# Performance work log

Hardware: AMD Instinct MI355X
Metric: run time of the kernel (lower is better)

Reference implementation:

```python
import jax, jax.numpy as jnp
import numpy as np

B, L1, C, L2, S, N_DB, N_CLS = 8, 1024, 128, 256, 16, 8192, 128
EPS = 1e-8


def setup_inputs() -> dict:
    key = jax.random.key(0)
    k1, k2, k3, k4 = jax.random.split(key, 4)
    seq_input = jax.random.randint(k1, (B, L1), 0, C)                      # token ids
    kp_indices = jnp.sort(jax.random.randint(k2, (B, S + 1), 0, L1), axis=-1)  # sorted keypoint positions
    database = jax.random.normal(k3, (N_DB, C, L2), dtype=jnp.float32)     # stored normalised snapshots
    db_classes = jax.random.randint(k4, (N_DB,), 0, N_CLS)                 # class label per db snapshot
    return {"seq_input": seq_input, "kp_indices": kp_indices,
            "database": database, "db_classes": db_classes}


def _snapshots(seq_input, kp_indices):
    # encodeContinuousVarsAsBits: one-hot bit encoding -> (B, L1, C)
    encoded = jax.nn.one_hot(seq_input, C, dtype=jnp.float32)
    # keypoint segments [start, end) per sliding window, resampled to length L2
    starts = kp_indices[:, :-1]                                            # (B, S)
    ends = jnp.maximum(kp_indices[:, 1:], starts + 1)                      # ensure end > start
    frac = (jnp.arange(L2, dtype=jnp.float32) + 0.5) / L2                  # (L2,)
    pos = starts[..., None].astype(jnp.float32) + \
          (ends - starts)[..., None].astype(jnp.float32) * frac            # (B, S, L2)
    idx = jnp.clip(pos.astype(jnp.int32), 0, L1 - 1)                       # gather indices
    b_idx = jnp.arange(B)[:, None, None]
    snaps = encoded[b_idx, idx, :]                                         # (B, S, L2, C)
    snaps = jnp.transpose(snaps, (0, 1, 3, 2))                             # (B, S, C, L2)
    return snaps.reshape(B * S, C, L2)


def reference(seq_input, kp_indices, database, db_classes):
    snaps = _snapshots(seq_input, kp_indices)                              # (B*S, C, L2)
    # removeInvalidNormalisedSnapshots: zero-mask all-zero snapshots (jit-safe analogue)
    nz = jnp.any(snaps != 0, axis=(1, 2))
    snaps = snaps * nz[:, None, None].astype(snaps.dtype)
    # compare_1d_batches: cosine similarity of flattened snapshots vs database
    a = snaps.reshape(B * S, C * L2)
    a = a / (jnp.linalg.norm(a, axis=-1, keepdims=True) + EPS)
    d = database.reshape(N_DB, C * L2)
    d = d / (jnp.linalg.norm(d, axis=-1, keepdims=True) + EPS)
    sims = a @ d.T                                                          # (B*S, N_DB)
    top = jnp.argmax(sims, axis=-1)
    predictions = db_classes[top]                                           # top_cls
    unit_sim = jnp.max(sims, axis=-1)
    return sims, predictions, unit_sim
```

## Files before the change

kernel.cpp:

```cpp
#include <hip/hip_runtime.h>
#include <stdint.h>

constexpr int kB   = 8;
constexpr int kL1  = 1024;
constexpr int kC   = 128;
constexpr int kL2  = 256;
constexpr int kS   = 16;
constexpr int kNQ  = kB * kS;
constexpr int kNDB = 8192;
constexpr float kEPS = 1e-8f;
constexpr int kRow = kC * kL2;

constexpr int kGrid = 256;
constexpr int kGens = kNDB / kGrid;

#define BARRIER_LG()                                          \
    do {                                                      \
        asm volatile("s_waitcnt lgkmcnt(0)" ::: "memory");    \
        __builtin_amdgcn_s_barrier();                         \
        asm volatile("" ::: "memory");                        \
    } while (0)

__global__ void build_table_kernel(const int* __restrict__ seq,
                                   const int* __restrict__ kp,
                                   uint32_t* __restrict__ table) {
    __shared__ int csh[kL2];
    const int q = blockIdx.x;
    const int s0 = threadIdx.x;
    const int b = q >> 4;
    const int s = q & 15;
    int start = kp[b * (kS + 1) + s];
    int end_  = kp[b * (kS + 1) + s + 1];
    if (end_ < start + 1) end_ = start + 1;
    {
        const int l2 = s0;
        const float frac = (l2 + 0.5f) * (1.0f / 256.0f);
        const float pos = __fadd_rn((float)start,
                                    __fmul_rn((float)(end_ - start), frac));
        int idx = (int)pos;
        idx = idx < 0 ? 0 : (idx > kL1 - 1 ? kL1 - 1 : idx);
        csh[l2] = seq[b * kL1 + idx];
    }
    __syncthreads();
    const int h = s0 >> 6;
    const int g = s0 & 63;
    const int l2r = h * 64 + (((q & 63) + g) & 63);
    const int c = csh[l2r];
    table[(q * 4 + h) * 64 + g] = (uint32_t)((c * kL2 + l2r) * 4);
}

__launch_bounds__(1024, 1)
__global__ void sim_kernel(const float* __restrict__ db,
                           const uint32_t* __restrict__ table,
                           float* __restrict__ sims) {
    __shared__ float tile[kRow];
    __shared__ float accp[2][3][128];
    __shared__ float nshp[2][8];

    const int blk  = blockIdx.x;
    const int row0 = blk * kGens;
    const int t = threadIdx.x;

    if (t < 512) {
        const int p = t;
        const float* rp = db + (size_t)row0 * kRow;
        float4 buf[16];
        #pragma unroll
        for (int k = 0; k < 16; ++k)
            buf[k] = *reinterpret_cast<const float4*>(rp + (p + 512 * k) * 4);

        #pragma unroll 1
        for (int j = 0; j < kGens; ++j) {
            float nr = 0.f;
            #pragma unroll
            for (int k = 0; k < 16; ++k) {
                const float4 v = buf[k];
                nr = fmaf(v.x, v.x, nr);
                nr = fmaf(v.y, v.y, nr);
                nr = fmaf(v.z, v.z, nr);
                nr = fmaf(v.w, v.w, nr);
                *reinterpret_cast<float4*>(&tile[(p + 512 * k) * 4]) = v;
            }
            #pragma unroll
            for (int off = 32; off > 0; off >>= 1) nr += __shfl_down(nr, off);
            if ((t & 63) == 0) nshp[j & 1][t >> 6] = nr;
            BARRIER_LG();

            if (j < kGens - 1) {
                const float* rpn = rp + kRow;
                #pragma unroll
                for (int k = 0; k < 16; ++k)
                    buf[k] = *reinterpret_cast<const float4*>(
                        rpn + (p + 512 * k) * 4);
                rp = rpn;
            }
            BARRIER_LG();
        }
    } else {
        const int u = t - 512;
        const int q = u & 127;
        const int h = u >> 7;
        float* simq = sims + (size_t)q * kNDB + row0;

        uint32_t adr[64];
        {
            const uint4* tp4 = reinterpret_cast<const uint4*>(
                table + (q * 4 + h) * 64);
            #pragma unroll
            for (int g4 = 0; g4 < 16; ++g4) {
                const uint4 v = tp4[g4];
                adr[g4 * 4 + 0] = v.x;
                adr[g4 * 4 + 1] = v.y;
                adr[g4 * 4 + 2] = v.z;
                adr[g4 * 4 + 3] = v.w;
            }
        }

        const char* tb = reinterpret_cast<const char*>(tile);
        float prev_part = 0.f;

        #pragma unroll 1
        for (int j = 0; j < kGens; ++j) {
            if (h == 0 && j > 0) {
                const int pj = (j - 1) & 1;
                const float total = prev_part + accp[pj][0][q] +
                                    accp[pj][1][q] + accp[pj][2][q];
                const float n2 =
                    ((nshp[pj][0] + nshp[pj][1]) + (nshp[pj][2] + nshp[pj][3])) +
                    ((nshp[pj][4] + nshp[pj][5]) + (nshp[pj][6] + nshp[pj][7]));
                const float inv = 1.0f / ((sqrtf(n2) + kEPS) * (16.0f + kEPS));
                simq[j - 1] = total * inv;
            }
            BARRIER_LG();

            float a[8];
            #pragma unroll
            for (int i = 0; i < 8; ++i) a[i] = 0.f;
            #pragma unroll
            for (int g = 0; g < 64; ++g)
                a[g & 7] += *reinterpret_cast<const float*>(tb + adr[g]);
            const float part = ((a[0] + a[1]) + (a[2] + a[3])) +
                               ((a[4] + a[5]) + (a[6] + a[7]));
            if (h) accp[j & 1][h - 1][q] = part;
            prev_part = part;
            BARRIER_LG();
        }
        if (h == 0) {
            const int pj = (kGens - 1) & 1;
            const float total = prev_part + accp[pj][0][q] +
                                accp[pj][1][q] + accp[pj][2][q];
            const float n2 =
                ((nshp[pj][0] + nshp[pj][1]) + (nshp[pj][2] + nshp[pj][3])) +
                ((nshp[pj][4] + nshp[pj][5]) + (nshp[pj][6] + nshp[pj][7]));
            const float inv = 1.0f / ((sqrtf(n2) + kEPS) * (16.0f + kEPS));
            simq[kGens - 1] = total * inv;
        }
    }
}

__global__ void argmax_kernel(const float* __restrict__ sims,
                              const int* __restrict__ db_classes,
                              float* __restrict__ preds,
                              float* __restrict__ unit) {
    const int q = blockIdx.x;
    const int t = threadIdx.x;
    const float* row = sims + (size_t)q * kNDB;

    float best = -1e30f;
    int bidx = kNDB;
    for (int n = t; n < kNDB; n += 256) {
        const float v = row[n];
        if (v > best) { best = v; bidx = n; }
    }

    __shared__ float bv[256];
    __shared__ int   bi[256];
    bv[t] = best;
    bi[t] = bidx;
    __syncthreads();
    for (int s2 = 128; s2 > 0; s2 >>= 1) {
        if (t < s2) {
            const float ov = bv[t + s2];
            const int   oi = bi[t + s2];
            if (ov > bv[t] || (ov == bv[t] && oi < bi[t])) {
                bv[t] = ov;
                bi[t] = oi;
            }
        }
        __syncthreads();
    }
    if (t == 0) {
        preds[q] = (float)db_classes[bi[0]];
        unit[q]  = bv[0];
    }
}

extern "C" void kernel_launch(void* const* d_in, const int* in_sizes, int n_in,
                              void* d_out, int out_size, void* d_ws, size_t ws_size,
                              hipStream_t stream) {
    const int*   seq        = (const int*)d_in[0];
    const int*   kp         = (const int*)d_in[1];
    const float* db         = (const float*)d_in[2];
    const int*   db_classes = (const int*)d_in[3];

    float* out   = (float*)d_out;
    float* preds = out + (size_t)kNQ * kNDB;
    float* unit  = preds + kNQ;

    uint32_t* table = (uint32_t*)d_ws;

    build_table_kernel<<<kNQ, kL2, 0, stream>>>(seq, kp, table);
    sim_kernel<<<kGrid, 1024, 0, stream>>>(db, table, out);
    argmax_kernel<<<kNQ, 256, 0, stream>>>(out, db_classes, preds, unit);
}
```

Measured before the change: 222.8 us.

## Split database row tile into double-buffered halves for load/gather overlap

The producer warps now stream each database row in two L2-column halves into a double-buffered shared-memory tile, writing the next half while consumers gather from the current one. Gather addresses are remapped to the half-tile layout, and each consumer group works only in the phase matching its half. The goal is to overlap global loads, LDS writes and gathers more finely and to halve the per-buffer LDS footprint. The cost is twice as many barrier phases, with only half the consumer warps active in each phase.

```diff
diff --git a/kernel.cpp b/kernel.cpp
--- a/kernel.cpp
+++ b/kernel.cpp
@@ -11,8 +11,10 @@
 constexpr float kEPS = 1e-8f;
 constexpr int kRow = kC * kL2;
 
-constexpr int kGrid = 256;
-constexpr int kGens = kNDB / kGrid;
+constexpr int kGrid  = 256;
+constexpr int kGens  = kNDB / kGrid;
+constexpr int kHalfF = kRow / 2;
+constexpr int kNPh   = 2 * kGens;
 
 #define BARRIER_LG()                                          \
     do {                                                      \
@@ -46,15 +48,39 @@
     const int g = s0 & 63;
     const int l2r = h * 64 + (((q & 63) + g) & 63);
     const int c = csh[l2r];
-    table[(q * 4 + h) * 64 + g] = (uint32_t)((c * kL2 + l2r) * 4);
+    table[(q * 4 + h) * 64 + g] = (uint32_t)((c * 128 + (l2r & 127)) * 4);
+}
+
+__device__ __forceinline__ void load_half(const float* __restrict__ rowp,
+                                          int hf, float4 (&buf)[8], int p) {
+    #pragma unroll
+    for (int k = 0; k < 8; ++k) {
+        const int f4 = p + 512 * k;
+        buf[k] = *reinterpret_cast<const float4*>(
+            rowp + (f4 >> 5) * kL2 + hf * 128 + (f4 & 31) * 4);
+    }
+}
+
+__device__ __forceinline__ void write_half(float* tp, const float4 (&buf)[8],
+                                           int p, float& nrm) {
+    #pragma unroll
+    for (int k = 0; k < 8; ++k) {
+        const int f4 = p + 512 * k;
+        const float4 v = buf[k];
+        nrm = fmaf(v.x, v.x, nrm);
+        nrm = fmaf(v.y, v.y, nrm);
+        nrm = fmaf(v.z, v.z, nrm);
+        nrm = fmaf(v.w, v.w, nrm);
+        *reinterpret_cast<float4*>(tp + f4 * 4) = v;
+    }
 }
 
 __launch_bounds__(1024, 1)
 __global__ void sim_kernel(const float* __restrict__ db,
                            const uint32_t* __restrict__ table,
                            float* __restrict__ sims) {
-    __shared__ float tile[kRow];
-    __shared__ float accp[2][3][128];
+    __shared__ float tile[2][kHalfF];
+    __shared__ float accp[2][4][128];
     __shared__ float nshp[2][8];
 
     const int blk  = blockIdx.x;
@@ -63,36 +89,30 @@
 
     if (t < 512) {
         const int p = t;
-        const float* rp = db + (size_t)row0 * kRow;
-        float4 buf[16];
-        #pragma unroll
-        for (int k = 0; k < 16; ++k)
-            buf[k] = *reinterpret_cast<const float4*>(rp + (p + 512 * k) * 4);
+        float4 buf[8];
+        float nrm = 0.f;
+        load_half(db + (size_t)row0 * kRow, 0, buf, p);
+        write_half(tile[0], buf, p, nrm);
+        load_half(db + (size_t)row0 * kRow, 1, buf, p);
+        BARRIER_LG();
 
         #pragma unroll 1
-        for (int j = 0; j < kGens; ++j) {
-            float nr = 0.f;
-            #pragma unroll
-            for (int k = 0; k < 16; ++k) {
-                const float4 v = buf[k];
-                nr = fmaf(v.x, v.x, nr);
-                nr = fmaf(v.y, v.y, nr);
-                nr = fmaf(v.z, v.z, nr);
-                nr = fmaf(v.w, v.w, nr);
-                *reinterpret_cast<float4*>(&tile[(p + 512 * k) * 4]) = v;
-            }
-            #pragma unroll
-            for (int off = 32; off > 0; off >>= 1) nr += __shfl_down(nr, off);
-            if ((t & 63) == 0) nshp[j & 1][t >> 6] = nr;
-            BARRIER_LG();
-
-            if (j < kGens - 1) {
-                const float* rpn = rp + kRow;
+        for (int ph = 0; ph < kNPh; ++ph) {
+            if (ph < kNPh - 1)
+                write_half(tile[(ph + 1) & 1], buf, p, nrm);
+
+            if ((ph & 1) == 0) {
+                float nw = nrm;
                 #pragma unroll
-                for (int k = 0; k < 16; ++k)
-                    buf[k] = *reinterpret_cast<const float4*>(
-                        rpn + (p + 512 * k) * 4);
-                rp = rpn;
+                for (int off = 32; off > 0; off >>= 1)
+                    nw += __shfl_down(nw, off);
+                if ((t & 63) == 0) nshp[(ph >> 1) & 1][t >> 6] = nw;
+                nrm = 0.f;
+            }
+
+            if (ph + 2 < kNPh) {
+                const int H = ph + 2;
+                load_half(db + (size_t)(row0 + (H >> 1)) * kRow, H & 1, buf, p);
             }
             BARRIER_LG();
         }
@@ -115,45 +135,44 @@
                 adr[g4 * 4 + 3] = v.w;
             }
         }
-
-        const char* tb = reinterpret_cast<const char*>(tile);
-        float prev_part = 0.f;
+        BARRIER_LG();
 
         #pragma unroll 1
-        for (int j = 0; j < kGens; ++j) {
-            if (h == 0 && j > 0) {
-                const int pj = (j - 1) & 1;
-                const float total = prev_part + accp[pj][0][q] +
-                                    accp[pj][1][q] + accp[pj][2][q];
+        for (int ph = 0; ph < kNPh; ++ph) {
+            if ((ph & 1) == 0 && h == 2 && ph >= 2) {
+                const int r = (ph - 2) >> 1, pj = r & 1;
+                const float total = (accp[pj][0][q] + accp[pj][1][q]) +
+                                    (accp[pj][2][q] + accp[pj][3][q]);
                 const float n2 =
                     ((nshp[pj][0] + nshp[pj][1]) + (nshp[pj][2] + nshp[pj][3])) +
                     ((nshp[pj][4] + nshp[pj][5]) + (nshp[pj][6] + nshp[pj][7]));
                 const float inv = 1.0f / ((sqrtf(n2) + kEPS) * (16.0f + kEPS));
-                simq[j - 1] = total * inv;
+                simq[r] = total * inv;
+            }
+
+            if ((ph & 1) == (h >> 1)) {
+                const char* tb = reinterpret_cast<const char*>(tile[ph & 1]);
+                float a[8];
+                #pragma unroll
+                for (int i = 0; i < 8; ++i) a[i] = 0.f;
+                #pragma unroll
+                for (int g = 0; g < 64; ++g)
+                    a[g & 7] += *reinterpret_cast<const float*>(tb + adr[g]);
+                accp[(ph >> 1) & 1][h][q] =
+                    ((a[0] + a[1]) + (a[2] + a[3])) +
+                    ((a[4] + a[5]) + (a[6] + a[7]));
             }
             BARRIER_LG();
-
-            float a[8];
-            #pragma unroll
-            for (int i = 0; i < 8; ++i) a[i] = 0.f;
-            #pragma unroll
-            for (int g = 0; g < 64; ++g)
-                a[g & 7] += *reinterpret_cast<const float*>(tb + adr[g]);
-            const float part = ((a[0] + a[1]) + (a[2] + a[3])) +
-                               ((a[4] + a[5]) + (a[6] + a[7]));
-            if (h) accp[j & 1][h - 1][q] = part;
-            prev_part = part;
-            BARRIER_LG();
-        }
-        if (h == 0) {
-            const int pj = (kGens - 1) & 1;
-            const float total = prev_part + accp[pj][0][q] +
-                                accp[pj][1][q] + accp[pj][2][q];
+        }
+        if (h == 2) {
+            const int r = kGens - 1, pj = r & 1;
+            const float total = (accp[pj][0][q] + accp[pj][1][q]) +
+                                (accp[pj][2][q] + accp[pj][3][q]);
             const float n2 =
                 ((nshp[pj][0] + nshp[pj][1]) + (nshp[pj][2] + nshp[pj][3])) +
                 ((nshp[pj][4] + nshp[pj][5]) + (nshp[pj][6] + nshp[pj][7]));
             const float inv = 1.0f / ((sqrtf(n2) + kEPS) * (16.0f + kEPS));
-            simq[kGens - 1] = total * inv;
+            simq[r] = total * inv;
         }
     }
 }
```

Result: no change. 222.5 us (-0.1%).
